# Kernel optimization log

Measured on AMD Instinct MI355X. Metric: run time of the kernel, lower is better.

The kernel has to match this reference:

```python
import jax, jax.numpy as jnp
import numpy as np

T = 2048
HIDDEN = 4096
H = 32
HKV = 8
D = 128
THETA = 10000.0


def setup_inputs() -> dict:
    key = jax.random.key(0)
    k1, k2, k3, k4, k5 = jax.random.split(key, 5)
    s = 0.02
    return {
        "x": jax.random.normal(k1, (T, 2 * HIDDEN), dtype=jnp.float32),
        "positions": jnp.arange(T, dtype=jnp.int32),
        "Wq": jax.random.normal(k2, (H * D, 2 * HIDDEN), dtype=jnp.float32) * s,
        "Wk": jax.random.normal(k3, (HKV * D, 2 * HIDDEN), dtype=jnp.float32) * s,
        "Wv": jax.random.normal(k4, (HKV * D, 2 * HIDDEN), dtype=jnp.float32) * s,
        "Wo": jax.random.normal(k5, (HIDDEN, H * D), dtype=jnp.float32) * s,
    }


def _rope_cos_sin(positions):
    # NeoX-style: cos_sin_cache[pos] = [cos(freqs), sin(freqs)], freqs over head_dim/2
    inv_freq = 1.0 / (THETA ** (jnp.arange(0, D, 2, dtype=jnp.float32) / D))
    freqs = positions.astype(jnp.float32)[:, None] * inv_freq  # [T, D/2]
    return jnp.cos(freqs)[:, None, :], jnp.sin(freqs)[:, None, :]  # broadcast over heads


def _apply_rope(t, cos, sin):
    half = D // 2
    t1, t2 = t[..., :half], t[..., half:]
    return jnp.concatenate([t1 * cos - t2 * sin, t2 * cos + t1 * sin], axis=-1)


def reference(x, positions, Wq, Wk, Wv, Wo):
    n = x.shape[0]
    q = (x @ Wq.T).reshape(n, H, D)
    k = (x @ Wk.T).reshape(n, HKV, D)
    v = (x @ Wv.T).reshape(n, HKV, D)
    cos, sin = _rope_cos_sin(positions)
    q = _apply_rope(q, cos, sin)
    k = _apply_rope(k, cos, sin)
    # cache starts empty -> k_full/v_full are just k/v; prefill (n>1) -> causal
    G = H // HKV  # GQA group size; avoid materializing repeated K/V
    qg = q.reshape(n, HKV, G, D)
    scale = D ** -0.5
    scores = jnp.einsum("tkgd,skd->kgts", qg, k) * scale  # [HKV, G, T, T]
    causal = jnp.arange(n)[:, None] >= jnp.arange(n)[None, :]
    scores = jnp.where(causal, scores, jnp.finfo(scores.dtype).min)
    p = jax.nn.softmax(scores, axis=-1)
    o = jnp.einsum("kgts,skd->tkgd", p, v).reshape(n, H * D)
    return o @ Wo.T
```

## Files before the change

kernel.cpp:

```cpp
#include <hip/hip_runtime.h>
#include <hip/hip_bf16.h>
#include <math.h>

typedef unsigned short u16;
typedef u16 u16x8 __attribute__((ext_vector_type(8)));
typedef __bf16 bf16x8 __attribute__((ext_vector_type(8)));
typedef float f32x4 __attribute__((ext_vector_type(4)));

#define T_SEQ 2048
#define IN_DIM 8192
#define QKV_COLS 6144
#define O_COLS 4096

__device__ __forceinline__ u16 f2bf(float f){
  unsigned u = __builtin_bit_cast(unsigned, f);
  u += 0x7fffu + ((u >> 16) & 1u);
  return (u16)(u >> 16);
}
__device__ __forceinline__ float bf2f(u16 h){
  unsigned u = ((unsigned)h) << 16;
  return __builtin_bit_cast(float, u);
}
__device__ __forceinline__ void gload16(const void* g, void* l){
  __builtin_amdgcn_global_load_lds((const __attribute__((address_space(1))) unsigned*)g,
                                   (__attribute__((address_space(3))) unsigned*)l, 16, 0, 0);
}
__device__ __forceinline__ void storeC(float* p, float v){ *p = v; }
__device__ __forceinline__ void storeC(u16* p, float v){ *p = f2bf(v); }

__global__ void cvt_all(const float* __restrict__ x, const float* __restrict__ wq,
                        const float* __restrict__ wk, const float* __restrict__ wv,
                        const float* __restrict__ wo,
                        u16* __restrict__ xb, u16* __restrict__ wb, u16* __restrict__ wob){
  const int NX  = T_SEQ*IN_DIM/4;
  const int NQ  = 4096*IN_DIM/4;
  const int NKV = 1024*IN_DIM/4;
  const int NO  = 4096*4096/4;
  const int TOT = NX + NQ + 2*NKV + NO;
  int stride = gridDim.x * blockDim.x;
  for (int i = blockIdx.x*blockDim.x + threadIdx.x; i < TOT; i += stride){
    const float4* s; ushort4* d; int j = i;
    if (j < NX){ s = (const float4*)x; d = (ushort4*)xb; }
    else { j -= NX;
      if (j < NQ){ s = (const float4*)wq; d = (ushort4*)wb; }
      else { j -= NQ;
        if (j < NKV){ s = (const float4*)wk; d = (ushort4*)(wb + (size_t)4096*IN_DIM); }
        else { j -= NKV;
          if (j < NKV){ s = (const float4*)wv; d = (ushort4*)(wb + (size_t)5120*IN_DIM); }
          else { j -= NKV; s = (const float4*)wo; d = (ushort4*)wob; } } } }
    float4 v = s[j];
    ushort4 o; o.x = f2bf(v.x); o.y = f2bf(v.y); o.z = f2bf(v.z); o.w = f2bf(v.w);
    d[j] = o;
  }
}

__global__ void rope_scale_kernel(u16* __restrict__ qkv, const int* __restrict__ pos){
  __shared__ float cs[64], sn[64];
  int t = blockIdx.x;
  int p = pos[t];
  if (threadIdx.x < 64){
    int i = threadIdx.x;
    double e = (double)(2*i) / 128.0;
    float invf = (float)pow(10000.0, -e);
    float ang = (float)p * invf;
    cs[i] = cosf(ang);
    sn[i] = sinf(ang);
  }
  __syncthreads();
  u16* row = qkv + (size_t)t * QKV_COLS;
  const float qscale = 0.08838834764831845f;
  for (int idx = threadIdx.x; idx < 40*64; idx += blockDim.x){
    int head = idx >> 6, i = idx & 63;
    int base = (head < 32) ? head*128 : 4096 + (head-32)*128;
    float sc = (head < 32) ? qscale : 1.0f;
    float t1 = bf2f(row[base + i]);
    float t2 = bf2f(row[base + i + 64]);
    row[base + i]      = f2bf((t1*cs[i] - t2*sn[i]) * sc);
    row[base + i + 64] = f2bf((t2*cs[i] + t1*sn[i]) * sc);
  }
}

template<typename OutT>
__global__ __launch_bounds__(512,2) void gemm_pipe(const u16* __restrict__ A, const u16* __restrict__ B,
                                                   OutT* __restrict__ C, int K, int ldc){
  __shared__ __attribute__((aligned(16))) u16 Asm[4*8192];
  __shared__ __attribute__((aligned(16))) u16 Bsm[4*8192];
  const int tid = threadIdx.x;
  const int w = tid >> 6, l = tid & 63;
  const int wm = w >> 2, wn = w & 3;
  const int lr = l & 15, lg = l >> 4;
  const int m0 = blockIdx.y * 256, n0 = blockIdx.x * 256;

  const int srow  = tid >> 2;
  const int sslot = ((tid & 3) - ((tid >> 3) & 3)) & 3;
  const u16* Ag = A + (size_t)(m0 + srow) * K + sslot * 8;
  const u16* Bg = B + (size_t)(n0 + srow) * K + sslot * 8;
  char* AsB = (char*)Asm;
  char* BsB = (char*)Bsm;
  const int sdst = w * 1024;

  int aoff[4], aoff2[4], boff[4];
  #pragma unroll
  for (int i = 0; i < 4; ++i){
    int ra = wm*128 + i*16 + lr;
    aoff[i]  = ra*64  + (((lg + (ra>>1)) & 3) << 4);
    int ra2 = wm*128 + 64 + i*16 + lr;
    aoff2[i] = ra2*64 + (((lg + (ra2>>1)) & 3) << 4);
    int rb = wn*64 + i*16 + lr;
    boff[i]  = rb*64  + (((lg + (rb>>1)) & 3) << 4);
  }

  f32x4 acc[8][4] = {};
  const int NT = K >> 5;

  #pragma unroll
  for (int t = 0; t < 2; ++t){
    gload16(Ag + t*32,                    AsB + t*16384 +        sdst);
    gload16(Ag + (size_t)128*K + t*32,    AsB + t*16384 + 8192 + sdst);
    gload16(Bg + t*32,                    BsB + t*16384 +        sdst);
    gload16(Bg + (size_t)128*K + t*32,    BsB + t*16384 + 8192 + sdst);
  }

  for (int t = 0; t < NT; ++t){
    const int bb = (t & 3) * 16384;
    if (t == NT-1) asm volatile("s_waitcnt vmcnt(0)" ::: "memory");
    else           asm volatile("s_waitcnt vmcnt(4)" ::: "memory");
    __builtin_amdgcn_s_barrier();
    bf16x8 bfr[4], afr[4];
    #pragma unroll
    for (int n = 0; n < 4; ++n) bfr[n] = *(const bf16x8*)(BsB + bb + boff[n]);
    #pragma unroll
    for (int i = 0; i < 4; ++i) afr[i] = *(const bf16x8*)(AsB + bb + aoff[i]);
    if (t + 2 < NT){
      const int nb = ((t+2) & 3) * 16384;
      gload16(Ag + (t+2)*32,                 AsB + nb +        sdst);
      gload16(Ag + (size_t)128*K + (t+2)*32, AsB + nb + 8192 + sdst);
    }
    __builtin_amdgcn_s_barrier();
    __builtin_amdgcn_s_setprio(1);
    #pragma unroll
    for (int i = 0; i < 4; ++i)
      #pragma unroll
      for (int n = 0; n < 4; ++n)
        acc[i][n] = __builtin_amdgcn_mfma_f32_16x16x32_bf16(afr[i], bfr[n], acc[i][n], 0, 0, 0);
    __builtin_amdgcn_s_setprio(0);
    bf16x8 afr2[4];
    #pragma unroll
    for (int i = 0; i < 4; ++i) afr2[i] = *(const bf16x8*)(AsB + bb + aoff2[i]);
    if (t + 2 < NT){
      const int nb = ((t+2) & 3) * 16384;
      gload16(Bg + (t+2)*32,                 BsB + nb +        sdst);
      gload16(Bg + (size_t)128*K + (t+2)*32, BsB + nb + 8192 + sdst);
    }
    __builtin_amdgcn_s_barrier();
    __builtin_amdgcn_s_setprio(1);
    #pragma unroll
    for (int i = 0; i < 4; ++i)
      #pragma unroll
      for (int n = 0; n < 4; ++n)
        acc[4+i][n] = __builtin_amdgcn_mfma_f32_16x16x32_bf16(afr2[i], bfr[n], acc[4+i][n], 0, 0, 0);
    __builtin_amdgcn_s_setprio(0);
  }

  #pragma unroll
  for (int m = 0; m < 8; ++m)
    #pragma unroll
    for (int n = 0; n < 4; ++n)
      #pragma unroll
      for (int r = 0; r < 4; ++r){
        int row = m0 + wm*128 + m*16 + lg*4 + r;
        int col = n0 + wn*64 + n*16 + lr;
        storeC(&C[(size_t)row*ldc + col], acc[m][n][r]);
      }
}

__global__ __launch_bounds__(256) void attn_kernel(const u16* __restrict__ qkv, u16* __restrict__ ob){
  __shared__ __attribute__((aligned(16))) u16 Ksm[32*128];
  __shared__ __attribute__((aligned(16))) u16 Vt[128*40];
  __shared__ __attribute__((aligned(16))) u16 Psm[4][32*40];
  const int tid = threadIdx.x, l = tid & 63, w = tid >> 6;
  const int lr = l & 15, lg = l >> 4;
  const int qb = (gridDim.x - 1) - blockIdx.x;
  const int kv = blockIdx.y;
  const int h = kv*4 + w;
  const int q0 = qb * 32;

  bf16x8 aq[2][4];
  #pragma unroll
  for (int mm = 0; mm < 2; ++mm)
    #pragma unroll
    for (int kk = 0; kk < 4; ++kk)
      aq[mm][kk] = *(const bf16x8*)(qkv + (size_t)(q0 + mm*16 + lr)*QKV_COLS + h*128 + kk*32 + lg*8);

  f32x4 oacc[2][8] = {};
  float mrun[2][4], lrun[2][4];
  #pragma unroll
  for (int mm=0;mm<2;mm++)
    #pragma unroll
    for (int r=0;r<4;r++){ mrun[mm][r] = -1e30f; lrun[mm][r] = 0.f; }

  const int cbv = ((tid & 15) << 4) | (tid >> 4);
  for (int kt = 0; kt <= qb; ++kt){
    const int s0 = kt * 32;
    #pragma unroll
    for (int i = 0; i < 2; ++i){
      int c = tid + i*256, s = c >> 4, dq = c & 15;
      u16x8 kvv = *(const u16x8*)(qkv + (size_t)(s0+s)*QKV_COLS + 4096 + kv*128 + dq*8);
      int lin = (s << 8) + (dq << 4); lin ^= (s & 7) << 4;
      *(u16x8*)((char*)Ksm + lin) = kvv;
    }
    #pragma unroll
    for (int i = 0; i < 2; ++i){
      int c = cbv + i*256, s = c >> 4, dq = c & 15;
      u16x8 vv = *(const u16x8*)(qkv + (size_t)(s0+s)*QKV_COLS + 5120 + kv*128 + dq*8);
      #pragma unroll
      for (int j = 0; j < 8; ++j) Vt[(dq*8+j)*40 + s] = vv[j];
    }
    __syncthreads();

    f32x4 sa[2][2] = {};
    #pragma unroll
    for (int kk = 0; kk < 4; ++kk){
      bf16x8 bk[2];
      #pragma unroll
      for (int nn = 0; nn < 2; ++nn){
        int srow = nn*16 + lr;
        int lin = (srow << 8) + (kk << 6) + (lg << 4); lin ^= (srow & 7) << 4;
        bk[nn] = *(const bf16x8*)((char*)Ksm + lin);
      }
      #pragma unroll
      for (int mm = 0; mm < 2; ++mm)
        #pragma unroll
        for (int nn = 0; nn < 2; ++nn)
          sa[mm][nn] = __builtin_amdgcn_mfma_f32_16x16x32_bf16(aq[mm][kk], bk[nn], sa[mm][nn], 0,0,0);
    }

    if (kt == qb){
      #pragma unroll
      for (int mm=0;mm<2;mm++)
        #pragma unroll
        for (int nn=0;nn<2;nn++)
          #pragma unroll
          for (int r=0;r<4;r++){
            int qrel = mm*16 + lg*4 + r, srel = nn*16 + lr;
            if (srel > qrel) sa[mm][nn][r] = -1e30f;
          }
    }

    float alph[2][4];
    #pragma unroll
    for (int mm=0;mm<2;mm++)
      #pragma unroll
      for (int r=0;r<4;r++){
        float v = fmaxf(sa[mm][0][r], sa[mm][1][r]);
        v = fmaxf(v, __shfl_xor(v, 1));
        v = fmaxf(v, __shfl_xor(v, 2));
        v = fmaxf(v, __shfl_xor(v, 4));
        v = fmaxf(v, __shfl_xor(v, 8));
        float mn = fmaxf(mrun[mm][r], v);
        float al = __expf(mrun[mm][r] - mn);
        float p0 = __expf(sa[mm][0][r] - mn);
        float p1 = __expf(sa[mm][1][r] - mn);
        sa[mm][0][r] = p0; sa[mm][1][r] = p1;
        float rs = p0 + p1;
        rs += __shfl_xor(rs, 1);
        rs += __shfl_xor(rs, 2);
        rs += __shfl_xor(rs, 4);
        rs += __shfl_xor(rs, 8);
        lrun[mm][r] = lrun[mm][r]*al + rs;
        mrun[mm][r] = mn;
        alph[mm][r] = al;
      }
    #pragma unroll
    for (int mm=0;mm<2;mm++)
      #pragma unroll
      for (int df=0;df<8;df++)
        #pragma unroll
        for (int r=0;r<4;r++)
          oacc[mm][df][r] *= alph[mm][r];

    #pragma unroll
    for (int mm=0;mm<2;mm++)
      #pragma unroll
      for (int nn=0;nn<2;nn++)
        #pragma unroll
        for (int r=0;r<4;r++)
          Psm[w][(mm*16 + lg*4 + r)*40 + nn*16 + lr] = f2bf(sa[mm][nn][r]);

    bf16x8 ap[2];
    #pragma unroll
    for (int mm=0;mm<2;mm++)
      ap[mm] = *(const bf16x8*)(&Psm[w][(mm*16 + lr)*40 + lg*8]);
    #pragma unroll
    for (int df=0;df<8;df++){
      bf16x8 bv = *(const bf16x8*)(&Vt[(df*16 + lr)*40 + lg*8]);
      #pragma unroll
      for (int mm=0;mm<2;mm++)
        oacc[mm][df] = __builtin_amdgcn_mfma_f32_16x16x32_bf16(ap[mm], bv, oacc[mm][df], 0,0,0);
    }
    __syncthreads();
  }

  #pragma unroll
  for (int mm=0;mm<2;mm++)
    #pragma unroll
    for (int df=0;df<8;df++)
      #pragma unroll
      for (int r=0;r<4;r++){
        float val = oacc[mm][df][r] / lrun[mm][r];
        int t = q0 + mm*16 + lg*4 + r;
        int col = h*128 + df*16 + lr;
        ob[(size_t)t*O_COLS + col] = f2bf(val);
      }
}

extern "C" void kernel_launch(void* const* d_in, const int* in_sizes, int n_in,
                              void* d_out, int out_size, void* d_ws, size_t ws_size,
                              hipStream_t stream){
  const float* x  = (const float*)d_in[0];
  const int*   pos= (const int*)d_in[1];
  const float* Wq = (const float*)d_in[2];
  const float* Wk = (const float*)d_in[3];
  const float* Wv = (const float*)d_in[4];
  const float* Wo = (const float*)d_in[5];
  float* out = (float*)d_out;

  char* ws = (char*)d_ws;
  u16* xb   = (u16*)(ws);
  u16* wb   = (u16*)(ws + 33554432);
  u16* wob  = (u16*)(ws + 134217728);
  u16* qkv  = (u16*)(ws + 167772160);
  u16* obuf = (u16*)(ws + 192937984);

  cvt_all<<<2048, 256, 0, stream>>>(x, Wq, Wk, Wv, Wo, xb, wb, wob);

  gemm_pipe<u16><<<dim3(24,8), 512, 0, stream>>>(xb, wb, qkv, IN_DIM, QKV_COLS);
  rope_scale_kernel<<<T_SEQ, 256, 0, stream>>>(qkv, pos);
  attn_kernel<<<dim3(64,8), 256, 0, stream>>>(qkv, obuf);
  gemm_pipe<float><<<dim3(16,8), 512, 0, stream>>>(obuf, wob, out, O_COLS, O_COLS);
}
```

Before: 919.1 us.

## Retile GEMMs to fill 256 CUs with narrower N tiles and single-barrier pipeline

The GEMM kernel is templated on the number of N fragments per wave, so the QKV projection uses 256x192 tiles and the output projection uses 256x128 tiles, each launching 256 blocks. The old grids had 192 and 128 blocks, which left CUs idle. The grid is now linearised with M as the fast index, so blocks that share a B tile sit next to each other. The inner loop now loads all eight A fragments at once and does one barrier per K step instead of two. In exchange, each tile does less compute per byte loaded, register pressure rises from the eight A fragments, and the vmcnt waits now depend on per-wave load counts.

```diff
diff --git a/kernel.cpp b/kernel.cpp
--- a/kernel.cpp
+++ b/kernel.cpp
@@ -80,96 +80,102 @@
   }
 }
 
-template<typename OutT>
+template<typename OutT, int NFRAG>
 __global__ __launch_bounds__(512,2) void gemm_pipe(const u16* __restrict__ A, const u16* __restrict__ B,
-                                                   OutT* __restrict__ C, int K, int ldc){
+                                                   OutT* __restrict__ C, int K, int ldc, int ntile_n){
   __shared__ __attribute__((aligned(16))) u16 Asm[4*8192];
-  __shared__ __attribute__((aligned(16))) u16 Bsm[4*8192];
+  __shared__ __attribute__((aligned(16))) u16 Bsm[4*NFRAG*2048];
   const int tid = threadIdx.x;
   const int w = tid >> 6, l = tid & 63;
   const int wm = w >> 2, wn = w & 3;
   const int lr = l & 15, lg = l >> 4;
-  const int m0 = blockIdx.y * 256, n0 = blockIdx.x * 256;
+  const int id = blockIdx.x;
+  const int m0 = (id & 7) * 256;
+  const int n0 = (id >> 3) * (NFRAG*64);
+  const int BBUF = NFRAG*4096;
 
   const int srow  = tid >> 2;
   const int sslot = ((tid & 3) - ((tid >> 3) & 3)) & 3;
-  const u16* Ag = A + (size_t)(m0 + srow) * K + sslot * 8;
-  const u16* Bg = B + (size_t)(n0 + srow) * K + sslot * 8;
+  const u16* Ag  = A + (size_t)(m0 + srow) * K + sslot * 8;
+  const u16* Bg  = B + (size_t)(n0 + srow) * K + sslot * 8;
+  const u16* Bg2 = B + (size_t)(n0 + 128 + srow) * K + sslot * 8;
   char* AsB = (char*)Asm;
   char* BsB = (char*)Bsm;
   const int sdst = w * 1024;
 
-  int aoff[4], aoff2[4], boff[4];
-  #pragma unroll
-  for (int i = 0; i < 4; ++i){
+  int aoff[8], boff[NFRAG];
+  #pragma unroll
+  for (int i = 0; i < 8; ++i){
     int ra = wm*128 + i*16 + lr;
-    aoff[i]  = ra*64  + (((lg + (ra>>1)) & 3) << 4);
-    int ra2 = wm*128 + 64 + i*16 + lr;
-    aoff2[i] = ra2*64 + (((lg + (ra2>>1)) & 3) << 4);
-    int rb = wn*64 + i*16 + lr;
-    boff[i]  = rb*64  + (((lg + (rb>>1)) & 3) << 4);
-  }
-
-  f32x4 acc[8][4] = {};
+    aoff[i] = ra*64 + (((lg + (ra>>1)) & 3) << 4);
+  }
+  #pragma unroll
+  for (int i = 0; i < NFRAG; ++i){
+    int rb = wn*(NFRAG*16) + i*16 + lr;
+    boff[i] = rb*64 + (((lg + (rb>>1)) & 3) << 4);
+  }
+
+  f32x4 acc[8][NFRAG];
+  #pragma unroll
+  for (int m = 0; m < 8; ++m)
+    #pragma unroll
+    for (int n = 0; n < NFRAG; ++n)
+      acc[m][n] = (f32x4){0.f,0.f,0.f,0.f};
+
   const int NT = K >> 5;
 
-  #pragma unroll
-  for (int t = 0; t < 2; ++t){
-    gload16(Ag + t*32,                    AsB + t*16384 +        sdst);
-    gload16(Ag + (size_t)128*K + t*32,    AsB + t*16384 + 8192 + sdst);
-    gload16(Bg + t*32,                    BsB + t*16384 +        sdst);
-    gload16(Bg + (size_t)128*K + t*32,    BsB + t*16384 + 8192 + sdst);
-  }
+  #define STAGE_TILE(tt) do { \
+    const int nb_ = ((tt) & 3); \
+    gload16(Ag + (tt)*32,                 AsB + nb_*16384 +        sdst); \
+    gload16(Ag + (size_t)128*K + (tt)*32, AsB + nb_*16384 + 8192 + sdst); \
+    gload16(Bg + (tt)*32,                 BsB + nb_*BBUF +         sdst); \
+    if (NFRAG == 3 && tid < 256) \
+      gload16(Bg2 + (tt)*32,              BsB + nb_*BBUF + 8192 +  sdst); \
+  } while(0)
+
+  STAGE_TILE(0);
+  STAGE_TILE(1);
 
   for (int t = 0; t < NT; ++t){
-    const int bb = (t & 3) * 16384;
-    if (t == NT-1) asm volatile("s_waitcnt vmcnt(0)" ::: "memory");
-    else           asm volatile("s_waitcnt vmcnt(4)" ::: "memory");
+    const int ab = (t & 3) * 16384;
+    const int bb = (t & 3) * BBUF;
+    if (t == NT-1){
+      asm volatile("s_waitcnt vmcnt(0)" ::: "memory");
+    } else if (NFRAG == 3){
+      if (w < 4) asm volatile("s_waitcnt vmcnt(4)" ::: "memory");
+      else       asm volatile("s_waitcnt vmcnt(3)" ::: "memory");
+    } else {
+      asm volatile("s_waitcnt vmcnt(3)" ::: "memory");
+    }
     __builtin_amdgcn_s_barrier();
-    bf16x8 bfr[4], afr[4];
-    #pragma unroll
-    for (int n = 0; n < 4; ++n) bfr[n] = *(const bf16x8*)(BsB + bb + boff[n]);
-    #pragma unroll
-    for (int i = 0; i < 4; ++i) afr[i] = *(const bf16x8*)(AsB + bb + aoff[i]);
-    if (t + 2 < NT){
-      const int nb = ((t+2) & 3) * 16384;
-      gload16(Ag + (t+2)*32,                 AsB + nb +        sdst);
-      gload16(Ag + (size_t)128*K + (t+2)*32, AsB + nb + 8192 + sdst);
-    }
-    __builtin_amdgcn_s_barrier();
+    __builtin_amdgcn_sched_barrier(0);
+
+    bf16x8 bfr[NFRAG], afr[8];
+    #pragma unroll
+    for (int n = 0; n < NFRAG; ++n) bfr[n] = *(const bf16x8*)(BsB + bb + boff[n]);
+    #pragma unroll
+    for (int i = 0; i < 8; ++i)     afr[i] = *(const bf16x8*)(AsB + ab + aoff[i]);
+
+    if (t + 2 < NT) STAGE_TILE(t+2);
+
     __builtin_amdgcn_s_setprio(1);
     #pragma unroll
-    for (int i = 0; i < 4; ++i)
-      #pragma unroll
-      for (int n = 0; n < 4; ++n)
+    for (int i = 0; i < 8; ++i)
+      #pragma unroll
+      for (int n = 0; n < NFRAG; ++n)
         acc[i][n] = __builtin_amdgcn_mfma_f32_16x16x32_bf16(afr[i], bfr[n], acc[i][n], 0, 0, 0);
     __builtin_amdgcn_s_setprio(0);
-    bf16x8 afr2[4];
-    #pragma unroll
-    for (int i = 0; i < 4; ++i) afr2[i] = *(const bf16x8*)(AsB + bb + aoff2[i]);
-    if (t + 2 < NT){
-      const int nb = ((t+2) & 3) * 16384;
-      gload16(Bg + (t+2)*32,                 BsB + nb +        sdst);
-      gload16(Bg + (size_t)128*K + (t+2)*32, BsB + nb + 8192 + sdst);
-    }
-    __builtin_amdgcn_s_barrier();
-    __builtin_amdgcn_s_setprio(1);
-    #pragma unroll
-    for (int i = 0; i < 4; ++i)
-      #pragma unroll
-      for (int n = 0; n < 4; ++n)
-        acc[4+i][n] = __builtin_amdgcn_mfma_f32_16x16x32_bf16(afr2[i], bfr[n], acc[4+i][n], 0, 0, 0);
-    __builtin_amdgcn_s_setprio(0);
-  }
+  }
+  #undef STAGE_TILE
 
   #pragma unroll
   for (int m = 0; m < 8; ++m)
     #pragma unroll
-    for (int n = 0; n < 4; ++n)
+    for (int n = 0; n < NFRAG; ++n)
       #pragma unroll
       for (int r = 0; r < 4; ++r){
         int row = m0 + wm*128 + m*16 + lg*4 + r;
-        int col = n0 + wn*64 + n*16 + lr;
+        int col = n0 + wn*(NFRAG*16) + n*16 + lr;
         storeC(&C[(size_t)row*ldc + col], acc[m][n][r]);
       }
 }
@@ -334,8 +340,8 @@
 
   cvt_all<<<2048, 256, 0, stream>>>(x, Wq, Wk, Wv, Wo, xb, wb, wob);
 
-  gemm_pipe<u16><<<dim3(24,8), 512, 0, stream>>>(xb, wb, qkv, IN_DIM, QKV_COLS);
+  gemm_pipe<u16,3><<<256, 512, 0, stream>>>(xb, wb, qkv, IN_DIM, QKV_COLS, 32);
   rope_scale_kernel<<<T_SEQ, 256, 0, stream>>>(qkv, pos);
   attn_kernel<<<dim3(64,8), 256, 0, stream>>>(qkv, obuf);
-  gemm_pipe<float><<<dim3(16,8), 512, 0, stream>>>(obuf, wob, out, O_COLS, O_COLS);
-}
+  gemm_pipe<float,2><<<256, 512, 0, stream>>>(obuf, wob, out, O_COLS, O_COLS, 32);
+}
```

After: 853.3 us. -7.2%, faster.
